# Kernel optimization log

Hardware: AMD Instinct MI355X
Metric: run time of the kernel (lower is better)

The kernel has to match this reference:

```python
import jax, jax.numpy as jnp
import numpy as np

BETA = 0.25


def _nearest(flat, cb):
    # flat: [N, D], cb: [K, D]
    dist = (jnp.sum(flat * flat, axis=1, keepdims=True)
            + jnp.sum(cb * cb, axis=1)
            - 2.0 * flat @ cb.T)  # [N, K]
    inds = jnp.argmin(dist, axis=1)  # [N]
    q = cb[inds]                     # gather == one_hot @ cb
    return q, inds


def _mse(a, b):
    d = a - b
    return jnp.mean(d * d)


def _closeness(latents, q_det, q_noisy=None):
    adj = q_det if q_noisy is None else q_noisy
    return (BETA * _mse(latents, jax.lax.stop_gradient(q_det))
            + _mse(adj, jax.lax.stop_gradient(latents)))


def setup_inputs() -> dict:
    key = jax.random.key(0)
    k1, k2, k3 = jax.random.split(key, 3)
    B, S, C, K, D = 8192, 64, 16, 8192, 1024
    x = jax.random.normal(k1, (B, S, C), dtype=jnp.float32)
    # codebooks initialized uniform(-1/K, 1/K) and mean-centered, as in initial_codebook
    inv = 1.0 / K
    in_cb = jax.random.uniform(k2, (K, D), dtype=jnp.float32, minval=-inv, maxval=inv)
    in_cb = in_cb - jnp.mean(in_cb, axis=0)
    out_cb = jax.random.uniform(k3, (K, D), dtype=jnp.float32, minval=-inv, maxval=inv)
    out_cb = out_cb - jnp.mean(out_cb, axis=0)
    return {"x": x, "in_codebook": in_cb, "out_codebook": out_cb}


def reference(x, in_codebook, out_codebook):
    B, S, C = x.shape
    flat = x.reshape(B, S * C)  # 'b s c -> b (s c)'
    # in-codebook quantization (noisy=False)
    x_q, x_inds = _nearest(flat, in_codebook)
    # reconstruct(encoding_inds): codebook gather (abstract in base class)
    recon = in_codebook[x_inds]
    # out-codebook quantization; noise_std = 0.0 so noisy inds == det inds
    rq_det, r_inds = _nearest(recon, out_codebook)
    rq_noisy = rq_det
    # straight-through output
    out = flat + jax.lax.stop_gradient(rq_noisy - flat)
    loss = (_closeness(flat, rq_det, rq_noisy)
            + _closeness(flat, x_q)
            + _closeness(recon, rq_det, rq_noisy))
    return out.reshape(B, S, C), loss
```

## Files before the change

### kernel.cpp

```cpp
#include <hip/hip_runtime.h>
#include <hip/hip_bf16.h>
#include <stdint.h>

#define N_ROWS 8192
#define DDIM   1024
#define KCB    8192

#define SX   (6.0f / 127.0f)
#define SCB  (1.3e-4f / 127.0f)
#define NS1  (1.0f / (SX  * SCB))
#define NS2  (1.0f / (SCB * SCB))

typedef int   int32x4 __attribute__((ext_vector_type(4)));

__device__ __forceinline__ int quant_pack4(float4 v, float inv) {
  int q0 = (int)rintf(fminf(fmaxf(v.x * inv, -127.f), 127.f));
  int q1 = (int)rintf(fminf(fmaxf(v.y * inv, -127.f), 127.f));
  int q2 = (int)rintf(fminf(fmaxf(v.z * inv, -127.f), 127.f));
  int q3 = (int)rintf(fminf(fmaxf(v.w * inv, -127.f), 127.f));
  return (q0 & 255) | ((q1 & 255) << 8) | ((q2 & 255) << 16) | (q3 << 24);
}

__global__ __launch_bounds__(256) void prep_x_i8(const float* __restrict__ x,
                                                 int* __restrict__ x8) {
  int i = blockIdx.x * 256 + threadIdx.x;
  float4 v = ((const float4*)x)[i];
  x8[i] = quant_pack4(v, 1.0f / SX);
}

__global__ __launch_bounds__(256) void prep_cb_i8(const float* __restrict__ cb,
                                                  int* __restrict__ cb8,
                                                  float* __restrict__ norms,
                                                  float norm_scale) {
  int r = blockIdx.x;
  int t = threadIdx.x;
  float4 v = ((const float4*)(cb + (size_t)r * DDIM))[t];
  cb8[(size_t)r * 256 + t] = quant_pack4(v, 1.0f / SCB);
  float s = v.x*v.x + v.y*v.y + v.z*v.z + v.w*v.w;
  #pragma unroll
  for (int sh = 32; sh > 0; sh >>= 1) s += __shfl_down(s, sh, 64);
  __shared__ float wsum[4];
  int lane = t & 63, w = t >> 6;
  if (lane == 0) wsum[w] = s;
  __syncthreads();
  if (t == 0) norms[r] = (wsum[0] + wsum[1] + wsum[2] + wsum[3]) * norm_scale;
}

#define BM 128
#define BN 128
#define BKB 64

#define AS1 __attribute__((address_space(1)))
#define AS3 __attribute__((address_space(3)))

__global__ __launch_bounds__(256) void gemm_argmin(
    const char* __restrict__ A0, const char* __restrict__ B0,
    const float* __restrict__ n0, unsigned long long* __restrict__ pk0,
    const char* __restrict__ A1, const char* __restrict__ B1,
    const float* __restrict__ n1, unsigned long long* __restrict__ pk1)
{
  __shared__ char As[2][BM * BKB];
  __shared__ char Bs[2][BN * BKB];

  const char* __restrict__ A     = blockIdx.z ? A1 : A0;
  const char* __restrict__ B     = blockIdx.z ? B1 : B0;
  const float* __restrict__ norms = blockIdx.z ? n1 : n0;
  unsigned long long* __restrict__ packed = blockIdx.z ? pk1 : pk0;

  const int t    = threadIdx.x;
  const int lane = t & 63;
  const int wid  = t >> 6;
  const int wr   = wid >> 1, wc = wid & 1;
  const int la   = lane & 15, lg = lane >> 4;
  const int brow = blockIdx.x * BM;
  const int bcol = blockIdx.y * BN;

  int srow[2], scol[2];
  #pragma unroll
  for (int i = 0; i < 2; ++i) {
    int c = i * 256 + t;
    srow[i] = c >> 2;
    int sl  = c & 3;
    scol[i] = ((sl ^ ((srow[i] >> 1) & 3)) << 4);
  }

  #define STAGE(tt, dA, dB) do {                                              \
    _Pragma("unroll")                                                         \
    for (int i = 0; i < 2; ++i) {                                             \
      int c = i * 256 + t;                                                    \
      const char* ga = A + (size_t)(brow + srow[i]) * DDIM + (tt) * BKB + scol[i]; \
      const char* gb = B + (size_t)(bcol + srow[i]) * DDIM + (tt) * BKB + scol[i]; \
      __builtin_amdgcn_global_load_lds((AS1 void*)ga, (AS3 void*)((dA) + c * 16), 16, 0, 0); \
      __builtin_amdgcn_global_load_lds((AS1 void*)gb, (AS3 void*)((dB) + c * 16), 16, 0, 0); \
    }                                                                         \
  } while (0)

  int aoff[4], boff[4];
  #pragma unroll
  for (int mi = 0; mi < 4; ++mi) {
    int r = wr * 64 + mi * 16 + la;
    aoff[mi] = r * BKB + ((lg ^ ((r >> 1) & 3)) << 4);
  }
  #pragma unroll
  for (int ni = 0; ni < 4; ++ni) {
    int r = wc * 64 + ni * 16 + la;
    boff[ni] = r * BKB + ((lg ^ ((r >> 1) & 3)) << 4);
  }

  int32x4 acc[4][4];
  #pragma unroll
  for (int i = 0; i < 4; ++i)
    #pragma unroll
    for (int j = 0; j < 4; ++j) acc[i][j] = (int32x4){0, 0, 0, 0};

  STAGE(0, As[0], Bs[0]);
  __syncthreads();

  int cur = 0;
  for (int kt = 0; kt < DDIM / BKB; ++kt) {
    if (kt < DDIM / BKB - 1) {
      if (cur) STAGE(kt + 1, As[0], Bs[0]);
      else     STAGE(kt + 1, As[1], Bs[1]);
    }
    const char* curA = As[cur];
    const char* curB = Bs[cur];
    int32x4 af[4], bfr[4];
    #pragma unroll
    for (int mi = 0; mi < 4; ++mi) af[mi]  = *(const int32x4*)(curA + aoff[mi]);
    #pragma unroll
    for (int ni = 0; ni < 4; ++ni) bfr[ni] = *(const int32x4*)(curB + boff[ni]);
    #pragma unroll
    for (int mi = 0; mi < 4; ++mi)
      #pragma unroll
      for (int ni = 0; ni < 4; ++ni)
        acc[mi][ni] = __builtin_amdgcn_mfma_i32_16x16x64_i8(af[mi], bfr[ni], acc[mi][ni], 0, 0, 0);
    __syncthreads();
    cur ^= 1;
  }
  #undef STAGE

  float nrm[4]; int colg[4];
  #pragma unroll
  for (int ni = 0; ni < 4; ++ni) {
    colg[ni] = bcol + wc * 64 + ni * 16 + la;
    nrm[ni]  = norms[colg[ni]];
  }
  #pragma unroll
  for (int mi = 0; mi < 4; ++mi) {
    #pragma unroll
    for (int j = 0; j < 4; ++j) {
      float best = nrm[0] - 2.0f * (float)acc[mi][0][j];
      int  bidx  = colg[0];
      #pragma unroll
      for (int ni = 1; ni < 4; ++ni) {
        float v = nrm[ni] - 2.0f * (float)acc[mi][ni][j];
        if (v < best || (v == best && colg[ni] < bidx)) { best = v; bidx = colg[ni]; }
      }
      #pragma unroll
      for (int s = 1; s < 16; s <<= 1) {
        float ov = __shfl_xor(best, s, 64);
        int   oi = __shfl_xor(bidx, s, 64);
        if (ov < best || (ov == best && oi < bidx)) { best = ov; bidx = oi; }
      }
      if (la == 0) {
        int row = brow + wr * 64 + mi * 16 + lg * 4 + j;
        unsigned int ub = __float_as_uint(best);
        ub = (ub & 0x80000000u) ? ~ub : (ub | 0x80000000u);
        unsigned long long pk = ((unsigned long long)ub << 32) | (unsigned int)bidx;
        atomicMin(packed + row, pk);
      }
    }
  }
}

__global__ __launch_bounds__(256) void finalize_k(const float* __restrict__ x,
                                                  const float* __restrict__ incb,
                                                  const float* __restrict__ outcb,
                                                  const unsigned long long* __restrict__ p1,
                                                  const unsigned long long* __restrict__ p2,
                                                  float* __restrict__ out,
                                                  double* __restrict__ accum) {
  int n  = blockIdx.x;
  int xi = (int)(p1[n] & 0xffffffffull);
  int ri = (int)(p2[xi] & 0xffffffffull);
  int t  = threadIdx.x;
  float4 f = ((const float4*)(x     + (size_t)n  * DDIM))[t];
  float4 a = ((const float4*)(incb  + (size_t)xi * DDIM))[t];
  float4 r = ((const float4*)(outcb + (size_t)ri * DDIM))[t];
  ((float4*)(out + (size_t)n * DDIM))[t] = r;
  float s = 0.f;
  { float d1 = f.x - r.x, d2 = f.x - a.x, d3 = a.x - r.x; s += d1*d1 + d2*d2 + d3*d3; }
  { float d1 = f.y - r.y, d2 = f.y - a.y, d3 = a.y - r.y; s += d1*d1 + d2*d2 + d3*d3; }
  { float d1 = f.z - r.z, d2 = f.z - a.z, d3 = a.z - r.z; s += d1*d1 + d2*d2 + d3*d3; }
  { float d1 = f.w - r.w, d2 = f.w - a.w, d3 = a.w - r.w; s += d1*d1 + d2*d2 + d3*d3; }
  #pragma unroll
  for (int sh = 32; sh > 0; sh >>= 1) s += __shfl_down(s, sh, 64);
  __shared__ float wsum[4];
  int lane = t & 63, w = t >> 6;
  if (lane == 0) wsum[w] = s;
  __syncthreads();
  if (t == 0) atomicAdd(accum, (double)(wsum[0] + wsum[1] + wsum[2] + wsum[3]));
}

__global__ void write_loss(const double* __restrict__ accum, float* __restrict__ loss_out) {
  *loss_out = (float)(1.25 * (*accum) / (double)((size_t)N_ROWS * DDIM));
}

extern "C" void kernel_launch(void* const* d_in, const int* in_sizes, int n_in,
                              void* d_out, int out_size, void* d_ws, size_t ws_size,
                              hipStream_t stream) {
  const float* x     = (const float*)d_in[0];
  const float* incb  = (const float*)d_in[1];
  const float* outcb = (const float*)d_in[2];
  float* out = (float*)d_out;
  char*  ws  = (char*)d_ws;
  const size_t MB = 1024 * 1024;

  char* flat8  = ws;
  char* incb8  = ws + 8  * MB;
  char* outcb8 = ws + 16 * MB;
  float* norms_in  = (float*)(ws + 24 * MB);
  float* norms_out = norms_in + KCB;
  unsigned long long* p1 = (unsigned long long*)(ws + 24 * MB + 64 * 1024);
  unsigned long long* p2 = p1 + N_ROWS;
  double* accum = (double*)(p2 + KCB);

  hipMemsetAsync(p1, 0xFF, (N_ROWS + KCB) * sizeof(unsigned long long), stream);
  hipMemsetAsync(accum, 0, sizeof(double), stream);

  prep_x_i8 <<<N_ROWS * DDIM / 1024, 256, 0, stream>>>(x, (int*)flat8);
  prep_cb_i8<<<KCB, 256, 0, stream>>>(incb,  (int*)incb8,  norms_in,  NS1);
  prep_cb_i8<<<KCB, 256, 0, stream>>>(outcb, (int*)outcb8, norms_out, NS2);

  gemm_argmin<<<dim3(N_ROWS / BM, KCB / BN, 2), 256, 0, stream>>>(
      flat8, incb8, norms_in,  p1,
      incb8, outcb8, norms_out, p2);

  finalize_k<<<N_ROWS, 256, 0, stream>>>(x, incb, outcb, p1, p2, out, accum);
  write_loss<<<1, 1, 0, stream>>>(accum, out + (size_t)N_ROWS * DDIM);
}
```

Baseline: 379.0 us.

## Triple-buffer GEMM LDS staging with vmcnt waits and merge prep kernels

The int8 GEMM-argmin main loop moves from double to triple buffering, prefetching two K-tiles ahead. It replaces __syncthreads with explicit s_waitcnt vmcnt plus raw s_barrier, so global loads stay in flight across a barrier. The three preprocessing kernels are also merged into one launch. LDS use grows by half, which may lower occupancy, and correctness now depends on the vmcnt counts matching how many loads STAGE issues.

```diff
diff --git a/kernel.cpp b/kernel.cpp
--- a/kernel.cpp
+++ b/kernel.cpp
@@ -21,19 +21,27 @@
   return (q0 & 255) | ((q1 & 255) << 8) | ((q2 & 255) << 16) | (q3 << 24);
 }
 
-__global__ __launch_bounds__(256) void prep_x_i8(const float* __restrict__ x,
-                                                 int* __restrict__ x8) {
-  int i = blockIdx.x * 256 + threadIdx.x;
-  float4 v = ((const float4*)x)[i];
-  x8[i] = quant_pack4(v, 1.0f / SX);
-}
-
-__global__ __launch_bounds__(256) void prep_cb_i8(const float* __restrict__ cb,
-                                                  int* __restrict__ cb8,
-                                                  float* __restrict__ norms,
-                                                  float norm_scale) {
-  int r = blockIdx.x;
+__global__ __launch_bounds__(256) void prep_all(const float* __restrict__ x,
+                                                const float* __restrict__ incb,
+                                                const float* __restrict__ outcb,
+                                                int* __restrict__ x8,
+                                                int* __restrict__ incb8,
+                                                int* __restrict__ outcb8,
+                                                float* __restrict__ norms_in,
+                                                float* __restrict__ norms_out) {
+  int b = blockIdx.x;
   int t = threadIdx.x;
+  if (b >= 2 * KCB) {
+    int i = (b - 2 * KCB) * 256 + t;
+    float4 v = ((const float4*)x)[i];
+    x8[i] = quant_pack4(v, 1.0f / SX);
+    return;
+  }
+  const float* cb = (b < KCB) ? incb : outcb;
+  int*  cb8       = (b < KCB) ? incb8 : outcb8;
+  float* norms    = (b < KCB) ? norms_in : norms_out;
+  float  nscale   = (b < KCB) ? NS1 : NS2;
+  int r = (b < KCB) ? b : b - KCB;
   float4 v = ((const float4*)(cb + (size_t)r * DDIM))[t];
   cb8[(size_t)r * 256 + t] = quant_pack4(v, 1.0f / SCB);
   float s = v.x*v.x + v.y*v.y + v.z*v.z + v.w*v.w;
@@ -43,15 +51,19 @@
   int lane = t & 63, w = t >> 6;
   if (lane == 0) wsum[w] = s;
   __syncthreads();
-  if (t == 0) norms[r] = (wsum[0] + wsum[1] + wsum[2] + wsum[3]) * norm_scale;
+  if (t == 0) norms[r] = (wsum[0] + wsum[1] + wsum[2] + wsum[3]) * nscale;
 }
 
 #define BM 128
 #define BN 128
 #define BKB 64
+#define NT  (DDIM / BKB)
 
 #define AS1 __attribute__((address_space(1)))
 #define AS3 __attribute__((address_space(3)))
+
+#define BAR() do { asm volatile("" ::: "memory"); __builtin_amdgcn_s_barrier(); \
+                   asm volatile("" ::: "memory"); } while (0)
 
 __global__ __launch_bounds__(256) void gemm_argmin(
     const char* __restrict__ A0, const char* __restrict__ B0,
@@ -59,8 +71,8 @@
     const char* __restrict__ A1, const char* __restrict__ B1,
     const float* __restrict__ n1, unsigned long long* __restrict__ pk1)
 {
-  __shared__ char As[2][BM * BKB];
-  __shared__ char Bs[2][BN * BKB];
+  __shared__ char As[3][BM * BKB];
+  __shared__ char Bs[3][BN * BKB];
 
   const char* __restrict__ A     = blockIdx.z ? A1 : A0;
   const char* __restrict__ B     = blockIdx.z ? B1 : B0;
@@ -114,16 +126,18 @@
     for (int j = 0; j < 4; ++j) acc[i][j] = (int32x4){0, 0, 0, 0};
 
   STAGE(0, As[0], Bs[0]);
-  __syncthreads();
-
-  int cur = 0;
-  for (int kt = 0; kt < DDIM / BKB; ++kt) {
-    if (kt < DDIM / BKB - 1) {
-      if (cur) STAGE(kt + 1, As[0], Bs[0]);
-      else     STAGE(kt + 1, As[1], Bs[1]);
+  STAGE(1, As[1], Bs[1]);
+  asm volatile("s_waitcnt vmcnt(4)" ::: "memory");
+  BAR();
+
+  for (int kt = 0; kt < NT; ++kt) {
+    int nx = kt + 2;
+    if (nx < NT) {
+      int bi = nx % 3;
+      STAGE(nx, As[bi], Bs[bi]);
     }
-    const char* curA = As[cur];
-    const char* curB = Bs[cur];
+    const char* curA = As[kt % 3];
+    const char* curB = Bs[kt % 3];
     int32x4 af[4], bfr[4];
     #pragma unroll
     for (int mi = 0; mi < 4; ++mi) af[mi]  = *(const int32x4*)(curA + aoff[mi]);
@@ -134,8 +148,8 @@
       #pragma unroll
       for (int ni = 0; ni < 4; ++ni)
         acc[mi][ni] = __builtin_amdgcn_mfma_i32_16x16x64_i8(af[mi], bfr[ni], acc[mi][ni], 0, 0, 0);
-    __syncthreads();
-    cur ^= 1;
+    if (kt < NT - 2)       { asm volatile("s_waitcnt vmcnt(4)" ::: "memory"); BAR(); }
+    else if (kt == NT - 2) { asm volatile("s_waitcnt vmcnt(0)" ::: "memory"); BAR(); }
   }
   #undef STAGE
 
@@ -228,9 +242,8 @@
   hipMemsetAsync(p1, 0xFF, (N_ROWS + KCB) * sizeof(unsigned long long), stream);
   hipMemsetAsync(accum, 0, sizeof(double), stream);
 
-  prep_x_i8 <<<N_ROWS * DDIM / 1024, 256, 0, stream>>>(x, (int*)flat8);
-  prep_cb_i8<<<KCB, 256, 0, stream>>>(incb,  (int*)incb8,  norms_in,  NS1);
-  prep_cb_i8<<<KCB, 256, 0, stream>>>(outcb, (int*)outcb8, norms_out, NS2);
+  prep_all<<<2 * KCB + N_ROWS * DDIM / 1024, 256, 0, stream>>>(
+      x, incb, outcb, (int*)flat8, (int*)incb8, (int*)outcb8, norms_in, norms_out);
 
   gemm_argmin<<<dim3(N_ROWS / BM, KCB / BN, 2), 256, 0, stream>>>(
       flat8, incb8, norms_in,  p1,
```

After: 352.0 us. 7.1% less time.
